# Performance work log

Hardware: AMD Instinct MI355X
Metric: run time of the kernel (lower is better)

The kernel has to match this reference:

```python
import jax, jax.numpy as jnp
import numpy as np

B, T, N = 16, 1024, 512        # batch, time tokens, neurons
DK_T, DK_S = 64, 128           # key dims (temporal, spatial)
# dim_T = N, dim_S = T, dim_value_T = N (required by cross einsum), heads = 1


def setup_inputs() -> dict:
    key = jax.random.key(0)
    ks = jax.random.split(key, 11)
    return {
        "x_T": jax.random.normal(ks[0], (B, T, N), jnp.float32),
        "x_S": jax.random.normal(ks[1], (B, N, T), jnp.float32),
        "Wq_T": jax.random.normal(ks[2], (N, DK_T), jnp.float32) * 0.05,
        "Wk_T": jax.random.normal(ks[3], (N, DK_T), jnp.float32) * 0.05,
        "Wv_T": jax.random.normal(ks[4], (N, N), jnp.float32) * 0.05,
        "Wq_S": jax.random.normal(ks[5], (T, DK_S), jnp.float32) * 0.05,
        "Wk_S": jax.random.normal(ks[6], (T, DK_S), jnp.float32) * 0.05,
        "Wout_T": jax.random.normal(ks[7], (N, N), jnp.float32) * 0.05,
        "bout_T": jax.random.normal(ks[8], (N,), jnp.float32) * 0.05,
        "bias_T": jax.random.normal(ks[9], (1, 1, 1, DK_T), jnp.float32),
        "bias_S": jax.random.normal(ks[10], (1, 1, 1, DK_S), jnp.float32),
    }


def reference(x_T, x_S, Wq_T, Wk_T, Wv_T, Wq_S, Wk_S, Wout_T, bout_T, bias_T, bias_S):
    scale_T = DK_T ** -0.5
    scale_S = DK_S ** -0.5
    # Temporal attention: tokens along time axis, heads=1 -> add h axis
    q_T = (x_T @ Wq_T)[:, None] * scale_T          # [b,1,t,dk_T]
    k_T = (x_T @ Wk_T)[:, None]                    # [b,1,t,dk_T]
    v_T = (x_T @ Wv_T)[:, None]                    # [b,1,t,n]  (dim_value_T = n)
    logits_T = jnp.einsum('bhid,bhjd->bhij', q_T + bias_T, k_T)  # [b,1,t,t]
    attn_T = jax.nn.softmax(logits_T, axis=-1)
    out_T = jnp.einsum('bhij,bhjd->bhid', attn_T, v_T)            # [b,1,t,n]
    # Spatial attention: tokens along neuron axis
    q_S = (x_S @ Wq_S)[:, None] * scale_S          # [b,1,n,dk_S]
    k_S = (x_S @ Wk_S)[:, None]                    # [b,1,n,dk_S]
    logits_S = jnp.einsum('bhid,bhjd->bhij', q_S + bias_S, k_S)   # [b,1,n,n]
    attn_S = jax.nn.softmax(logits_S, axis=-1)
    # spatial_temporal_1 cross combination: attn_S mixes the neuron axis of out_T
    out_T = jnp.einsum('bhij,bhtj->bhti', attn_S, out_T)          # [b,1,t,n]
    out_T = out_T.reshape(B, T, N)                 # 'b h t d -> b t (h d)'
    out_T = out_T @ Wout_T + bout_T                # to_out_T
    return jnp.transpose(out_T, (0, 2, 1))         # [b, n, t]
```

## Files before the change

kernel.cpp:

```cpp
#include <hip/hip_runtime.h>
#include <cstddef>

typedef short short8 __attribute__((ext_vector_type(8)));
typedef unsigned short ushortx8 __attribute__((ext_vector_type(8)));
typedef float floatx4 __attribute__((ext_vector_type(4)));

__device__ __forceinline__ unsigned int bf16_rne(float x) {
    unsigned int u = __float_as_uint(x);
    return (u + 0x7fffu + ((u >> 16) & 1u)) >> 16;
}

__device__ __forceinline__ void split4(const floatx4 v,
                                       unsigned long long& hp,
                                       unsigned long long& lp) {
    unsigned int h[4], l[4];
    #pragma unroll
    for (int j = 0; j < 4; ++j) {
        h[j] = bf16_rne(v[j]);
        float hf = __uint_as_float(h[j] << 16);
        l[j] = bf16_rne(v[j] - hf);
    }
    hp = (unsigned long long)(h[0] | (h[1] << 16)) |
         ((unsigned long long)(h[2] | (h[3] << 16)) << 32);
    lp = (unsigned long long)(l[0] | (l[1] << 16)) |
         ((unsigned long long)(l[2] | (l[3] << 16)) << 32);
}

__device__ __forceinline__ unsigned long long pack_hi4(const floatx4 v) {
    unsigned int h0 = bf16_rne(v[0]), h1 = bf16_rne(v[1]);
    unsigned int h2 = bf16_rne(v[2]), h3 = bf16_rne(v[3]);
    return (unsigned long long)(h0 | (h1 << 16)) |
           ((unsigned long long)(h2 | (h3 << 16)) << 32);
}

template<int BM, int BN, int AMODE, int BMODE, int OUTMODE, bool HASBIAS>
__global__ __launch_bounds__(256, 2)
void gemm_nt(const void* __restrict__ Ah_, const void* __restrict__ Al_,
             const void* __restrict__ Bh_, const void* __restrict__ Bl_,
             void* __restrict__ C_, void* __restrict__ Cl_,
             const float* __restrict__ bias,
             int K, int lda, int ldb, int ldc,
             long sA, long sB, long sC, float alpha, int nsplit)
{
    constexpr bool ALO = (AMODE == 1 || AMODE == 3);
    constexpr bool BLO = (BMODE == 1 || BMODE == 3);
    constexpr int LS = 40;
    __shared__ unsigned short Ash[2][BM][LS];
    __shared__ unsigned short Als[2][ALO ? BM : 1][LS];
    __shared__ unsigned short Bsh[2][BN][LS];
    __shared__ unsigned short Bls[2][BLO ? BN : 1][LS];

    const unsigned int gx = gridDim.x;
    const unsigned int nwg = gx * gridDim.y;
    unsigned int flat = blockIdx.y * gx + blockIdx.x;
    {
        unsigned int qq = nwg >> 3, rr = nwg & 7;
        unsigned int xcd = flat & 7, idx = flat >> 3;
        flat = (xcd < rr) ? (xcd * (qq + 1) + idx)
                          : (rr * (qq + 1) + (xcd - rr) * qq + idx);
    }
    const int b   = blockIdx.z;
    const int bm0 = (flat / gx) * BM;
    const int bn0 = (flat % gx) * BN;
    const int tid  = threadIdx.x;
    const int lane = tid & 63;
    const int wid  = tid >> 6;
    const int wr = wid >> 1, wc = wid & 1;
    constexpr int WM = BM / 2, WN = BN / 2;
    constexpr int FM = WM / 16, FN = WN / 16;
    floatx4 acc[FM][FN] = {};
    const int l15  = lane & 15;
    const int koff = (lane >> 4) * 8;

    constexpr int ACHF = BM * 32 / 4, NAF0 = (ACHF + 255) / 256;
    constexpr int ACHH = BM * 32 / 8, NAH0 = (ACHH + 255) / 256;
    constexpr int BCHF = BN * 32 / 4, NBF0 = (BCHF + 255) / 256;
    constexpr int BCHH = BN * 32 / 8, NBH0 = (BCHH + 255) / 256;
    constexpr int NAF = (AMODE <= 1) ? NAF0 : 1;
    constexpr int NAH = (AMODE >= 2) ? NAH0 : 1;
    constexpr int NBF = (BMODE <= 1) ? NBF0 : 1;
    constexpr int NBH = (BMODE >= 2) ? NBH0 : 1;
    floatx4  aF[NAF], bF[NBF];
    ushortx8 aH[NAH], aL[NAH], bH[NBH], bL[NBH];

    auto loadA = [&](int k0) {
        if (AMODE <= 1) {
            const float* A = (const float*)Ah_ + (long)b * sA;
            #pragma unroll
            for (int i = 0; i < NAF; ++i) {
                int idx = i * 256 + tid;
                if (ACHF % 256 == 0 || idx < ACHF) {
                    int flatc = idx * 4;
                    int r = flatc >> 5, c = flatc & 31;
                    aF[i] = *(const floatx4*)(A + (long)(bm0 + r) * lda + k0 + c);
                }
            }
        } else {
            const unsigned short* A  = (const unsigned short*)Ah_ + (long)b * sA;
            const unsigned short* Al = (const unsigned short*)Al_ + (long)b * sA;
            #pragma unroll
            for (int i = 0; i < NAH; ++i) {
                int idx = i * 256 + tid;
                if (ACHH % 256 == 0 || idx < ACHH) {
                    int flatc = idx * 8;
                    int r = flatc >> 5, c = flatc & 31;
                    aH[i] = *(const ushortx8*)(A + (long)(bm0 + r) * lda + k0 + c);
                    if (AMODE == 3)
                        aL[i] = *(const ushortx8*)(Al + (long)(bm0 + r) * lda + k0 + c);
                }
            }
        }
    };
    auto loadB = [&](int k0) {
        if (BMODE <= 1) {
            const float* Bp = (const float*)Bh_ + (long)b * sB;
            #pragma unroll
            for (int i = 0; i < NBF; ++i) {
                int idx = i * 256 + tid;
                if (BCHF % 256 == 0 || idx < BCHF) {
                    int flatc = idx * 4;
                    int r = flatc >> 5, c = flatc & 31;
                    bF[i] = *(const floatx4*)(Bp + (long)(bn0 + r) * ldb + k0 + c);
                }
            }
        } else {
            const unsigned short* Bp = (const unsigned short*)Bh_ + (long)b * sB;
            const unsigned short* Bl = (const unsigned short*)Bl_ + (long)b * sB;
            #pragma unroll
            for (int i = 0; i < NBH; ++i) {
                int idx = i * 256 + tid;
                if (BCHH % 256 == 0 || idx < BCHH) {
                    int flatc = idx * 8;
                    int r = flatc >> 5, c = flatc & 31;
                    bH[i] = *(const ushortx8*)(Bp + (long)(bn0 + r) * ldb + k0 + c);
                    if (BMODE == 3)
                        bL[i] = *(const ushortx8*)(Bl + (long)(bn0 + r) * ldb + k0 + c);
                }
            }
        }
    };
    auto writeA = [&](int bf) {
        if (AMODE <= 1) {
            #pragma unroll
            for (int i = 0; i < NAF; ++i) {
                int idx = i * 256 + tid;
                if (ACHF % 256 == 0 || idx < ACHF) {
                    int flatc = idx * 4;
                    int r = flatc >> 5, c = flatc & 31;
                    if (AMODE == 1) {
                        unsigned long long hp, lp; split4(aF[i], hp, lp);
                        *(unsigned long long*)&Ash[bf][r][c] = hp;
                        *(unsigned long long*)&Als[bf][r][c] = lp;
                    } else {
                        *(unsigned long long*)&Ash[bf][r][c] = pack_hi4(aF[i]);
                    }
                }
            }
        } else {
            #pragma unroll
            for (int i = 0; i < NAH; ++i) {
                int idx = i * 256 + tid;
                if (ACHH % 256 == 0 || idx < ACHH) {
                    int flatc = idx * 8;
                    int r = flatc >> 5, c = flatc & 31;
                    *(ushortx8*)&Ash[bf][r][c] = aH[i];
                    if (AMODE == 3) *(ushortx8*)&Als[bf][r][c] = aL[i];
                }
            }
        }
    };
    auto writeB = [&](int bf) {
        if (BMODE <= 1) {
            #pragma unroll
            for (int i = 0; i < NBF; ++i) {
                int idx = i * 256 + tid;
                if (BCHF % 256 == 0 || idx < BCHF) {
                    int flatc = idx * 4;
                    int r = flatc >> 5, c = flatc & 31;
                    if (BMODE == 1) {
                        unsigned long long hp, lp; split4(bF[i], hp, lp);
                        *(unsigned long long*)&Bsh[bf][r][c] = hp;
                        *(unsigned long long*)&Bls[bf][r][c] = lp;
                    } else {
                        *(unsigned long long*)&Bsh[bf][r][c] = pack_hi4(bF[i]);
                    }
                }
            }
        } else {
            #pragma unroll
            for (int i = 0; i < NBH; ++i) {
                int idx = i * 256 + tid;
                if (BCHH % 256 == 0 || idx < BCHH) {
                    int flatc = idx * 8;
                    int r = flatc >> 5, c = flatc & 31;
                    *(ushortx8*)&Bsh[bf][r][c] = bH[i];
                    if (BMODE == 3) *(ushortx8*)&Bls[bf][r][c] = bL[i];
                }
            }
        }
    };
    auto compute = [&](int bf) {
        short8 ah[FM], al[FM], bh[FN], bl[FN];
        #pragma unroll
        for (int mi = 0; mi < FM; ++mi) {
            ah[mi] = *(const short8*)&Ash[bf][wr * WM + mi * 16 + l15][koff];
            if (ALO) al[mi] = *(const short8*)&Als[bf][wr * WM + mi * 16 + l15][koff];
        }
        #pragma unroll
        for (int ni = 0; ni < FN; ++ni) {
            bh[ni] = *(const short8*)&Bsh[bf][wc * WN + ni * 16 + l15][koff];
            if (BLO) bl[ni] = *(const short8*)&Bls[bf][wc * WN + ni * 16 + l15][koff];
        }
        #pragma unroll
        for (int mi = 0; mi < FM; ++mi)
            #pragma unroll
            for (int ni = 0; ni < FN; ++ni) {
                if (ALO)
                    acc[mi][ni] = __builtin_amdgcn_mfma_f32_16x16x32_bf16(
                        al[mi], bh[ni], acc[mi][ni], 0, 0, 0);
                if (BLO)
                    acc[mi][ni] = __builtin_amdgcn_mfma_f32_16x16x32_bf16(
                        ah[mi], bl[ni], acc[mi][ni], 0, 0, 0);
                acc[mi][ni] = __builtin_amdgcn_mfma_f32_16x16x32_bf16(
                    ah[mi], bh[ni], acc[mi][ni], 0, 0, 0);
            }
    };

    loadA(0); loadB(0);
    writeA(0); writeB(0);
    __syncthreads();
    int cur = 0;
    for (int k0 = 32; k0 < K; k0 += 32) {
        loadA(k0); loadB(k0);
        compute(cur);
        writeA(cur ^ 1); writeB(cur ^ 1);
        __syncthreads();
        cur ^= 1;
    }
    compute(cur);

    const int rq = (lane >> 4) * 4;
    #pragma unroll
    for (int mi = 0; mi < FM; ++mi) {
        #pragma unroll
        for (int ni = 0; ni < FN; ++ni) {
            int gm = bm0 + wr * WM + mi * 16 + rq;
            int gn = bn0 + wc * WN + ni * 16 + l15;
            float ae = (gn < nsplit) ? alpha : 1.0f;
            float be = 0.f;
            if (HASBIAS) be = (gn < nsplit) ? bias[gn] : 0.0f;
            float vals[4];
            #pragma unroll
            for (int j = 0; j < 4; ++j) vals[j] = acc[mi][ni][j] * ae + be;
            if (OUTMODE == 0) {
                float* C = (float*)C_ + (long)b * sC;
                #pragma unroll
                for (int j = 0; j < 4; ++j) C[(long)(gm + j) * ldc + gn] = vals[j];
            } else if (OUTMODE == 1) {
                float* C = (float*)C_ + (long)b * sC;
                floatx4 o;
                #pragma unroll
                for (int j = 0; j < 4; ++j) o[j] = vals[j];
                *(floatx4*)(C + (long)gn * ldc + gm) = o;
            } else if (OUTMODE == 2) {
                unsigned short* Ch = (unsigned short*)C_ + (long)b * sC;
                unsigned short* Cl = (unsigned short*)Cl_ + (long)b * sC;
                #pragma unroll
                for (int j = 0; j < 4; ++j) {
                    unsigned int h = bf16_rne(vals[j]);
                    float hf = __uint_as_float(h << 16);
                    unsigned int lo = bf16_rne(vals[j] - hf);
                    Ch[(long)(gm + j) * ldc + gn] = (unsigned short)h;
                    Cl[(long)(gm + j) * ldc + gn] = (unsigned short)lo;
                }
            } else {
                unsigned short* Ch = (unsigned short*)C_ + (long)b * sC;
                #pragma unroll
                for (int j = 0; j < 4; ++j)
                    Ch[(long)(gm + j) * ldc + gn] = (unsigned short)bf16_rne(vals[j]);
            }
        }
    }
}

template<int COLS, int DK, int LDQK>
__global__ __launch_bounds__(256, 2)
void qk_softmax(const unsigned short* __restrict__ qk_h,
                const unsigned short* __restrict__ qk_l,
                unsigned short* __restrict__ P)
{
    constexpr int WCOLS = COLS / 4;
    constexpr int FN = WCOLS / 16;
    constexpr int QPAD = DK + 24;
    __shared__ unsigned short Qh[32][QPAD];
    __shared__ unsigned short Ql[32][QPAD];
    __shared__ float red[32][4];
    __shared__ unsigned short Pl[32][COLS + 8];

    const int b  = blockIdx.y;
    const int q0 = blockIdx.x * 32;
    const long rowBase = (long)b * COLS;
    const int tid = threadIdx.x;
    const int lane = tid & 63, wid = tid >> 6;
    const int l15 = lane & 15, g = lane >> 4;
    const int koff = g * 8;

    constexpr int QCH = DK / 8;
    for (int i = tid; i < 32 * QCH; i += 256) {
        int r = i / QCH, c = (i % QCH) * 8;
        *(ushortx8*)&Qh[r][c] = *(const ushortx8*)(qk_h + (rowBase + q0 + r) * LDQK + c);
        *(ushortx8*)&Ql[r][c] = *(const ushortx8*)(qk_l + (rowBase + q0 + r) * LDQK + c);
    }
    __syncthreads();

    floatx4 acc[2][FN] = {};
    const unsigned short* kh = qk_h + rowBase * LDQK + DK;
    const unsigned short* kl = qk_l + rowBase * LDQK + DK;

    #pragma unroll
    for (int kk = 0; kk < DK; kk += 32) {
        short8 ah[2], al[2];
        #pragma unroll
        for (int mi = 0; mi < 2; ++mi) {
            ah[mi] = *(const short8*)&Qh[mi * 16 + l15][kk + koff];
            al[mi] = *(const short8*)&Ql[mi * 16 + l15][kk + koff];
        }
        #pragma unroll
        for (int ni = 0; ni < FN; ++ni) {
            long krow = wid * WCOLS + ni * 16 + l15;
            short8 bh = *(const short8*)(kh + krow * LDQK + kk + koff);
            short8 bl = *(const short8*)(kl + krow * LDQK + kk + koff);
            #pragma unroll
            for (int mi = 0; mi < 2; ++mi) {
                acc[mi][ni] = __builtin_amdgcn_mfma_f32_16x16x32_bf16(al[mi], bh, acc[mi][ni], 0, 0, 0);
                acc[mi][ni] = __builtin_amdgcn_mfma_f32_16x16x32_bf16(ah[mi], bl, acc[mi][ni], 0, 0, 0);
                acc[mi][ni] = __builtin_amdgcn_mfma_f32_16x16x32_bf16(ah[mi], bh, acc[mi][ni], 0, 0, 0);
            }
        }
    }

    float pm[2][4];
    #pragma unroll
    for (int mi = 0; mi < 2; ++mi)
        #pragma unroll
        for (int j = 0; j < 4; ++j) {
            float m = acc[mi][0][j];
            #pragma unroll
            for (int ni = 1; ni < FN; ++ni) m = fmaxf(m, acc[mi][ni][j]);
            pm[mi][j] = m;
        }
    #pragma unroll
    for (int msk = 1; msk < 16; msk <<= 1) {
        #pragma unroll
        for (int mi = 0; mi < 2; ++mi)
            #pragma unroll
            for (int j = 0; j < 4; ++j)
                pm[mi][j] = fmaxf(pm[mi][j], __shfl_xor(pm[mi][j], msk));
    }
    if (l15 == 0) {
        #pragma unroll
        for (int mi = 0; mi < 2; ++mi)
            #pragma unroll
            for (int j = 0; j < 4; ++j) red[mi * 16 + g * 4 + j][wid] = pm[mi][j];
    }
    __syncthreads();
    float rm[2][4];
    #pragma unroll
    for (int mi = 0; mi < 2; ++mi)
        #pragma unroll
        for (int j = 0; j < 4; ++j) {
            const float* r4 = red[mi * 16 + g * 4 + j];
            rm[mi][j] = fmaxf(fmaxf(r4[0], r4[1]), fmaxf(r4[2], r4[3]));
        }
    __syncthreads();

    float ps[2][4] = {};
    #pragma unroll
    for (int mi = 0; mi < 2; ++mi)
        #pragma unroll
        for (int ni = 0; ni < FN; ++ni)
            #pragma unroll
            for (int j = 0; j < 4; ++j) {
                float e = __expf(acc[mi][ni][j] - rm[mi][j]);
                acc[mi][ni][j] = e;
                ps[mi][j] += e;
            }
    #pragma unroll
    for (int msk = 1; msk < 16; msk <<= 1) {
        #pragma unroll
        for (int mi = 0; mi < 2; ++mi)
            #pragma unroll
            for (int j = 0; j < 4; ++j)
                ps[mi][j] += __shfl_xor(ps[mi][j], msk);
    }
    if (l15 == 0) {
        #pragma unroll
        for (int mi = 0; mi < 2; ++mi)
            #pragma unroll
            for (int j = 0; j < 4; ++j) red[mi * 16 + g * 4 + j][wid] = ps[mi][j];
    }
    __syncthreads();
    float inv[2][4];
    #pragma unroll
    for (int mi = 0; mi < 2; ++mi)
        #pragma unroll
        for (int j = 0; j < 4; ++j) {
            const float* r4 = red[mi * 16 + g * 4 + j];
            inv[mi][j] = 1.0f / (r4[0] + r4[1] + r4[2] + r4[3]);
        }

    #pragma unroll
    for (int mi = 0; mi < 2; ++mi)
        #pragma unroll
        for (int ni = 0; ni < FN; ++ni)
            #pragma unroll
            for (int j = 0; j < 4; ++j)
                Pl[mi * 16 + g * 4 + j][wid * WCOLS + ni * 16 + l15] =
                    (unsigned short)bf16_rne(acc[mi][ni][j] * inv[mi][j]);
    __syncthreads();

    constexpr int PCH = COLS / 8;
    for (int i = tid; i < 32 * PCH; i += 256) {
        int r = i / PCH, c = (i % PCH) * 8;
        *(ushortx8*)(P + (rowBase + q0 + r) * COLS + c) = *(const ushortx8*)&Pl[r][c];
    }
}

__global__ __launch_bounds__(256)
void transpose_split(const float* __restrict__ in,
                     unsigned short* __restrict__ outH,
                     unsigned short* __restrict__ outL,
                     int R, int C, int rowOff, int ldo)
{
    __shared__ float tile[32][33];
    const int tc = blockIdx.x * 32, tr = blockIdx.y * 32;
    const int x = threadIdx.x, y = threadIdx.y;
    #pragma unroll
    for (int i = 0; i < 32; i += 8)
        tile[y + i][x] = in[(long)(tr + y + i) * C + tc + x];
    __syncthreads();
    #pragma unroll
    for (int i = 0; i < 32; i += 8) {
        float v = tile[x][y + i];
        unsigned int h = bf16_rne(v);
        float hf = __uint_as_float(h << 16);
        unsigned int lo = bf16_rne(v - hf);
        long idx = (long)(tc + y + i + rowOff) * ldo + tr + x;
        outH[idx] = (unsigned short)h;
        outL[idx] = (unsigned short)lo;
    }
}

extern "C" void kernel_launch(void* const* d_in, const int* in_sizes, int n_in,
                              void* d_out, int out_size, void* d_ws, size_t ws_size,
                              hipStream_t stream)
{
    (void)in_sizes; (void)n_in; (void)out_size; (void)ws_size;
    const float* x_T    = (const float*)d_in[0];
    const float* x_S    = (const float*)d_in[1];
    const float* Wq_T   = (const float*)d_in[2];
    const float* Wk_T   = (const float*)d_in[3];
    const float* Wv_T   = (const float*)d_in[4];
    const float* Wq_S   = (const float*)d_in[5];
    const float* Wk_S   = (const float*)d_in[6];
    const float* Wout_T = (const float*)d_in[7];
    const float* bout_T = (const float*)d_in[8];
    const float* bias_T = (const float*)d_in[9];
    const float* bias_S = (const float*)d_in[10];
    float* out = (float*)d_out;

    constexpr int B = 16, T = 1024, N = 512, DKT = 64, DKS = 128;
    typedef unsigned short us;

    char* w = (char*)d_ws;
    size_t off = 0;
    auto alloc = [&](size_t bytes) { char* p = w + off; off = (off + bytes + 255) & ~(size_t)255; return p; };
    us* wqkT_h = (us*)alloc(128 * 512 * 2);
    us* wqkT_l = (us*)alloc(128 * 512 * 2);
    us* wvt_h  = (us*)alloc(512 * 512 * 2);
    us* wvt_l  = (us*)alloc(512 * 512 * 2);
    us* wqks_h = (us*)alloc(256 * 1024 * 2);
    us* wqks_l = (us*)alloc(256 * 1024 * 2);
    us* wout_h = (us*)alloc(512 * 512 * 2);
    us* wout_l = (us*)alloc(512 * 512 * 2);
    us* qk_h   = (us*)alloc((size_t)16384 * 128 * 2);
    us* qk_l   = (us*)alloc((size_t)16384 * 128 * 2);
    us* P_T    = (us*)alloc((size_t)B * T * T * 2);
    us* P_S    = (us*)alloc((size_t)B * N * N * 2);
    us* vT_h   = (us*)alloc((size_t)B * N * T * 2);
    us* vT_l   = (us*)alloc((size_t)B * N * T * 2);
    us* outT_h = (us*)alloc((size_t)B * T * N * 2);
    us* outT_l = (us*)alloc((size_t)B * T * N * 2);
    us* out2_h = vT_h;
    us* out2_l = vT_l;

    const float scale_T = 0.125f;
    const float scale_S = 0.088388347648318447f;
    const int BIG = 1 << 30;

    dim3 tb(32, 8);
    transpose_split<<<dim3(2, 16),  tb, 0, stream>>>(Wq_T,   wqkT_h, wqkT_l, 512, 64,   0, 512);
    transpose_split<<<dim3(2, 16),  tb, 0, stream>>>(Wk_T,   wqkT_h, wqkT_l, 512, 64,  64, 512);
    transpose_split<<<dim3(16, 16), tb, 0, stream>>>(Wv_T,   wvt_h,  wvt_l,  512, 512,  0, 512);
    transpose_split<<<dim3(4, 32),  tb, 0, stream>>>(Wq_S,   wqks_h, wqks_l, 1024, 128, 0, 1024);
    transpose_split<<<dim3(4, 32),  tb, 0, stream>>>(Wk_S,   wqks_h, wqks_l, 1024, 128, 128, 1024);
    transpose_split<<<dim3(16, 16), tb, 0, stream>>>(Wout_T, wout_h, wout_l, 512, 512,  0, 512);

    gemm_nt<32, 128, 1, 3, 2, true><<<dim3(1, 512, 1), 256, 0, stream>>>(
        x_T, nullptr, wqkT_h, wqkT_l, qk_h, qk_l, bias_T,
        512, 512, 512, 128, 0, 0, 0, scale_T, 64);
    gemm_nt<128, 128, 3, 0, 3, false><<<dim3(8, 4, B), 256, 0, stream>>>(
        wvt_h, wvt_l, x_T, nullptr, vT_h, nullptr, nullptr,
        512, 512, 512, 1024, 0, (long)T * N, (long)N * T, 1.0f, 0);
    qk_softmax<1024, 64, 128><<<dim3(32, 16), 256, 0, stream>>>(qk_h, qk_l, P_T);
    gemm_nt<128, 128, 2, 2, 2, false><<<dim3(4, 8, B), 256, 0, stream>>>(
        P_T, nullptr, vT_h, nullptr, outT_h, outT_l, nullptr,
        1024, 1024, 1024, 512, (long)T * T, (long)N * T, (long)T * N, 1.0f, 0);

    gemm_nt<32, 128, 1, 3, 2, true><<<dim3(2, 256, 1), 256, 0, stream>>>(
        x_S, nullptr, wqks_h, wqks_l, qk_h, qk_l, bias_S,
        1024, 1024, 1024, 256, 0, 0, 0, scale_S, 128);
    qk_softmax<512, 128, 256><<<dim3(16, 16), 256, 0, stream>>>(qk_h, qk_l, P_S);
    gemm_nt<128, 128, 3, 2, 2, false><<<dim3(4, 8, B), 256, 0, stream>>>(
        outT_h, outT_l, P_S, nullptr, out2_h, out2_l, nullptr,
        512, 512, 512, 512, (long)T * N, (long)N * N, (long)T * N, 1.0f, 0);
    gemm_nt<128, 128, 3, 2, 1, true><<<dim3(4, 8, B), 256, 0, stream>>>(
        out2_h, out2_l, wout_h, nullptr, out, nullptr, bout_T,
        512, 512, 512, 1024, (long)T * N, 0, (long)N * T, 1.0f, BIG);
}
```

Baseline: 221.8 us.

## Reassociate spatial mixing with output projection, pre-split inputs, shrink GEMM tiles

Transposes P_S in the softmax epilogue and first multiplies it with Wout_T, a per-batch 512x512 product. Applying that merged matrix to out_T removes one full T×N×N GEMM per batch. It also adds a convert_split pass that turns x_T and x_S into bf16 hi/lo arrays once, so the projection GEMMs read split data instead of converting inside the loads. Tiles shrink to 64x64 or 64x128, occupancy is raised to 4 blocks per SM, and the batch index is folded into a flat 2D grid, all to give more waves. The merged matrix M1t is stored only as the bf16 high part, which may lower accuracy.

```diff
diff --git a/kernel.cpp b/kernel.cpp
--- a/kernel.cpp
+++ b/kernel.cpp
@@ -3,6 +3,7 @@
 
 typedef short short8 __attribute__((ext_vector_type(8)));
 typedef unsigned short ushortx8 __attribute__((ext_vector_type(8)));
+typedef unsigned short ushortx4 __attribute__((ext_vector_type(4)));
 typedef float floatx4 __attribute__((ext_vector_type(4)));
 
 __device__ __forceinline__ unsigned int bf16_rne(float x) {
@@ -33,14 +34,36 @@
            ((unsigned long long)(h2 | (h3 << 16)) << 32);
 }
 
+__global__ __launch_bounds__(256)
+void convert_split(const float* __restrict__ in, long n,
+                   unsigned short* __restrict__ H, unsigned short* __restrict__ L)
+{
+    long n4 = n >> 2;
+    for (long i = (long)blockIdx.x * 256 + threadIdx.x; i < n4;
+         i += (long)gridDim.x * 256) {
+        long e = i << 2;
+        floatx4 v = *(const floatx4*)(in + e);
+        ushortx4 h4, l4;
+        #pragma unroll
+        for (int j = 0; j < 4; ++j) {
+            unsigned int h = bf16_rne(v[j]);
+            float hf = __uint_as_float(h << 16);
+            h4[j] = (unsigned short)h;
+            l4[j] = (unsigned short)bf16_rne(v[j] - hf);
+        }
+        *(ushortx4*)(H + e) = h4;
+        *(ushortx4*)(L + e) = l4;
+    }
+}
+
 template<int BM, int BN, int AMODE, int BMODE, int OUTMODE, bool HASBIAS>
-__global__ __launch_bounds__(256, 2)
+__global__ __launch_bounds__(256, 4)
 void gemm_nt(const void* __restrict__ Ah_, const void* __restrict__ Al_,
              const void* __restrict__ Bh_, const void* __restrict__ Bl_,
              void* __restrict__ C_, void* __restrict__ Cl_,
              const float* __restrict__ bias,
              int K, int lda, int ldb, int ldc,
-             long sA, long sB, long sC, float alpha, int nsplit)
+             long sA, long sB, long sC, float alpha, int nsplit, int mtiles)
 {
     constexpr bool ALO = (AMODE == 1 || AMODE == 3);
     constexpr bool BLO = (BMODE == 1 || BMODE == 3);
@@ -59,9 +82,11 @@
         flat = (xcd < rr) ? (xcd * (qq + 1) + idx)
                           : (rr * (qq + 1) + (xcd - rr) * qq + idx);
     }
-    const int b   = blockIdx.z;
-    const int bm0 = (flat / gx) * BM;
-    const int bn0 = (flat % gx) * BN;
+    const unsigned int perb = gx * (unsigned int)mtiles;
+    const int b   = flat / perb;
+    const unsigned int rm = flat % perb;
+    const int bm0 = (rm / gx) * BM;
+    const int bn0 = (rm % gx) * BN;
     const int tid  = threadIdx.x;
     const int lane = tid & 63;
     const int wid  = tid >> 6;
@@ -90,8 +115,7 @@
             for (int i = 0; i < NAF; ++i) {
                 int idx = i * 256 + tid;
                 if (ACHF % 256 == 0 || idx < ACHF) {
-                    int flatc = idx * 4;
-                    int r = flatc >> 5, c = flatc & 31;
+                    int fc = idx * 4; int r = fc >> 5, c = fc & 31;
                     aF[i] = *(const floatx4*)(A + (long)(bm0 + r) * lda + k0 + c);
                 }
             }
@@ -102,8 +126,7 @@
             for (int i = 0; i < NAH; ++i) {
                 int idx = i * 256 + tid;
                 if (ACHH % 256 == 0 || idx < ACHH) {
-                    int flatc = idx * 8;
-                    int r = flatc >> 5, c = flatc & 31;
+                    int fc = idx * 8; int r = fc >> 5, c = fc & 31;
                     aH[i] = *(const ushortx8*)(A + (long)(bm0 + r) * lda + k0 + c);
                     if (AMODE == 3)
                         aL[i] = *(const ushortx8*)(Al + (long)(bm0 + r) * lda + k0 + c);
@@ -118,8 +141,7 @@
             for (int i = 0; i < NBF; ++i) {
                 int idx = i * 256 + tid;
                 if (BCHF % 256 == 0 || idx < BCHF) {
-                    int flatc = idx * 4;
-                    int r = flatc >> 5, c = flatc & 31;
+                    int fc = idx * 4; int r = fc >> 5, c = fc & 31;
                     bF[i] = *(const floatx4*)(Bp + (long)(bn0 + r) * ldb + k0 + c);
                 }
             }
@@ -130,8 +152,7 @@
             for (int i = 0; i < NBH; ++i) {
                 int idx = i * 256 + tid;
                 if (BCHH % 256 == 0 || idx < BCHH) {
-                    int flatc = idx * 8;
-                    int r = flatc >> 5, c = flatc & 31;
+                    int fc = idx * 8; int r = fc >> 5, c = fc & 31;
                     bH[i] = *(const ushortx8*)(Bp + (long)(bn0 + r) * ldb + k0 + c);
                     if (BMODE == 3)
                         bL[i] = *(const ushortx8*)(Bl + (long)(bn0 + r) * ldb + k0 + c);
@@ -145,8 +166,7 @@
             for (int i = 0; i < NAF; ++i) {
                 int idx = i * 256 + tid;
                 if (ACHF % 256 == 0 || idx < ACHF) {
-                    int flatc = idx * 4;
-                    int r = flatc >> 5, c = flatc & 31;
+                    int fc = idx * 4; int r = fc >> 5, c = fc & 31;
                     if (AMODE == 1) {
                         unsigned long long hp, lp; split4(aF[i], hp, lp);
                         *(unsigned long long*)&Ash[bf][r][c] = hp;
@@ -161,8 +181,7 @@
             for (int i = 0; i < NAH; ++i) {
                 int idx = i * 256 + tid;
                 if (ACHH % 256 == 0 || idx < ACHH) {
-                    int flatc = idx * 8;
-                    int r = flatc >> 5, c = flatc & 31;
+                    int fc = idx * 8; int r = fc >> 5, c = fc & 31;
                     *(ushortx8*)&Ash[bf][r][c] = aH[i];
                     if (AMODE == 3) *(ushortx8*)&Als[bf][r][c] = aL[i];
                 }
@@ -175,8 +194,7 @@
             for (int i = 0; i < NBF; ++i) {
                 int idx = i * 256 + tid;
                 if (BCHF % 256 == 0 || idx < BCHF) {
-                    int flatc = idx * 4;
-                    int r = flatc >> 5, c = flatc & 31;
+                    int fc = idx * 4; int r = fc >> 5, c = fc & 31;
                     if (BMODE == 1) {
                         unsigned long long hp, lp; split4(bF[i], hp, lp);
                         *(unsigned long long*)&Bsh[bf][r][c] = hp;
@@ -191,8 +209,7 @@
             for (int i = 0; i < NBH; ++i) {
                 int idx = i * 256 + tid;
                 if (BCHH % 256 == 0 || idx < BCHH) {
-                    int flatc = idx * 8;
-                    int r = flatc >> 5, c = flatc & 31;
+                    int fc = idx * 8; int r = fc >> 5, c = fc & 31;
                     *(ushortx8*)&Bsh[bf][r][c] = bH[i];
                     if (BMODE == 3) *(ushortx8*)&Bls[bf][r][c] = bL[i];
                 }
@@ -283,7 +300,7 @@
     }
 }
 
-template<int COLS, int DK, int LDQK>
+template<int COLS, int DK, int LDQK, bool TRANSP>
 __global__ __launch_bounds__(256, 2)
 void qk_softmax(const unsigned short* __restrict__ qk_h,
                 const unsigned short* __restrict__ qk_l,
@@ -419,10 +436,21 @@
                     (unsigned short)bf16_rne(acc[mi][ni][j] * inv[mi][j]);
     __syncthreads();
 
-    constexpr int PCH = COLS / 8;
-    for (int i = tid; i < 32 * PCH; i += 256) {
-        int r = i / PCH, c = (i % PCH) * 8;
-        *(ushortx8*)(P + (rowBase + q0 + r) * COLS + c) = *(const ushortx8*)&Pl[r][c];
+    if (TRANSP) {
+        for (int i = tid; i < COLS * 4; i += 256) {
+            int c = i >> 2;
+            int rc = (i & 3) * 8;
+            ushortx8 v;
+            #pragma unroll
+            for (int s = 0; s < 8; ++s) v[s] = Pl[rc + s][c];
+            *(ushortx8*)(P + (rowBase + c) * COLS + q0 + rc) = v;
+        }
+    } else {
+        constexpr int PCH = COLS / 8;
+        for (int i = tid; i < 32 * PCH; i += 256) {
+            int r = i / PCH, c = (i % PCH) * 8;
+            *(ushortx8*)(P + (rowBase + q0 + r) * COLS + c) = *(const ushortx8*)&Pl[r][c];
+        }
     }
 }
 
@@ -486,17 +514,19 @@
     us* qk_h   = (us*)alloc((size_t)16384 * 128 * 2);
     us* qk_l   = (us*)alloc((size_t)16384 * 128 * 2);
     us* P_T    = (us*)alloc((size_t)B * T * T * 2);
-    us* P_S    = (us*)alloc((size_t)B * N * N * 2);
+    us* P_St   = (us*)alloc((size_t)B * N * N * 2);
     us* vT_h   = (us*)alloc((size_t)B * N * T * 2);
     us* vT_l   = (us*)alloc((size_t)B * N * T * 2);
     us* outT_h = (us*)alloc((size_t)B * T * N * 2);
     us* outT_l = (us*)alloc((size_t)B * T * N * 2);
-    us* out2_h = vT_h;
-    us* out2_l = vT_l;
+    us* x_h    = (us*)alloc((size_t)16384 * 512 * 2);
+    us* x_l    = (us*)alloc((size_t)16384 * 512 * 2);
+    us* M1t_h  = vT_l;
 
     const float scale_T = 0.125f;
     const float scale_S = 0.088388347648318447f;
     const int BIG = 1 << 30;
+    const long XE = (long)16384 * 512;
 
     dim3 tb(32, 8);
     transpose_split<<<dim3(2, 16),  tb, 0, stream>>>(Wq_T,   wqkT_h, wqkT_l, 512, 64,   0, 512);
@@ -506,25 +536,27 @@
     transpose_split<<<dim3(4, 32),  tb, 0, stream>>>(Wk_S,   wqks_h, wqks_l, 1024, 128, 128, 1024);
     transpose_split<<<dim3(16, 16), tb, 0, stream>>>(Wout_T, wout_h, wout_l, 512, 512,  0, 512);
 
-    gemm_nt<32, 128, 1, 3, 2, true><<<dim3(1, 512, 1), 256, 0, stream>>>(
-        x_T, nullptr, wqkT_h, wqkT_l, qk_h, qk_l, bias_T,
-        512, 512, 512, 128, 0, 0, 0, scale_T, 64);
-    gemm_nt<128, 128, 3, 0, 3, false><<<dim3(8, 4, B), 256, 0, stream>>>(
-        wvt_h, wvt_l, x_T, nullptr, vT_h, nullptr, nullptr,
-        512, 512, 512, 1024, 0, (long)T * N, (long)N * T, 1.0f, 0);
-    qk_softmax<1024, 64, 128><<<dim3(32, 16), 256, 0, stream>>>(qk_h, qk_l, P_T);
-    gemm_nt<128, 128, 2, 2, 2, false><<<dim3(4, 8, B), 256, 0, stream>>>(
+    convert_split<<<2048, 256, 0, stream>>>(x_T, XE, x_h, x_l);
+    gemm_nt<64, 64, 3, 3, 2, true><<<dim3(2, 256), 256, 0, stream>>>(
+        x_h, x_l, wqkT_h, wqkT_l, qk_h, qk_l, bias_T,
+        512, 512, 512, 128, 0, 0, 0, scale_T, 64, 256);
+    gemm_nt<64, 128, 3, 2, 3, false><<<dim3(8, 8 * B), 256, 0, stream>>>(
+        wvt_h, wvt_l, x_h, nullptr, vT_h, nullptr, nullptr,
+        512, 512, 512, 1024, 0, (long)T * N, (long)N * T, 1.0f, 0, 8);
+    qk_softmax<1024, 64, 128, false><<<dim3(32, 16), 256, 0, stream>>>(qk_h, qk_l, P_T);
+    gemm_nt<64, 128, 2, 2, 2, false><<<dim3(4, 16 * B), 256, 0, stream>>>(
         P_T, nullptr, vT_h, nullptr, outT_h, outT_l, nullptr,
-        1024, 1024, 1024, 512, (long)T * T, (long)N * T, (long)T * N, 1.0f, 0);
-
-    gemm_nt<32, 128, 1, 3, 2, true><<<dim3(2, 256, 1), 256, 0, stream>>>(
-        x_S, nullptr, wqks_h, wqks_l, qk_h, qk_l, bias_S,
-        1024, 1024, 1024, 256, 0, 0, 0, scale_S, 128);
-    qk_softmax<512, 128, 256><<<dim3(16, 16), 256, 0, stream>>>(qk_h, qk_l, P_S);
-    gemm_nt<128, 128, 3, 2, 2, false><<<dim3(4, 8, B), 256, 0, stream>>>(
-        outT_h, outT_l, P_S, nullptr, out2_h, out2_l, nullptr,
-        512, 512, 512, 512, (long)T * N, (long)N * N, (long)T * N, 1.0f, 0);
-    gemm_nt<128, 128, 3, 2, 1, true><<<dim3(4, 8, B), 256, 0, stream>>>(
-        out2_h, out2_l, wout_h, nullptr, out, nullptr, bout_T,
-        512, 512, 512, 1024, (long)T * N, 0, (long)N * T, 1.0f, BIG);
-}
+        1024, 1024, 1024, 512, (long)T * T, (long)N * T, (long)T * N, 1.0f, 0, 16);
+
+    convert_split<<<2048, 256, 0, stream>>>(x_S, XE, x_h, x_l);
+    gemm_nt<64, 64, 3, 3, 2, true><<<dim3(4, 128), 256, 0, stream>>>(
+        x_h, x_l, wqks_h, wqks_l, qk_h, qk_l, bias_S,
+        1024, 1024, 1024, 256, 0, 0, 0, scale_S, 128, 128);
+    qk_softmax<512, 128, 256, true><<<dim3(16, 16), 256, 0, stream>>>(qk_h, qk_l, P_St);
+    gemm_nt<64, 128, 3, 2, 3, false><<<dim3(4, 8 * B), 256, 0, stream>>>(
+        wout_h, wout_l, P_St, nullptr, M1t_h, nullptr, nullptr,
+        512, 512, 512, 512, 0, (long)N * N, (long)N * N, 1.0f, 0, 8);
+    gemm_nt<64, 128, 3, 2, 1, true><<<dim3(4, 16 * B), 256, 0, stream>>>(
+        outT_h, outT_l, M1t_h, nullptr, out, nullptr, bout_T,
+        512, 512, 512, 1024, (long)T * N, (long)N * N, (long)N * T, 1.0f, BIG, 16);
+}
```

Measured after the change: 223.9 us. About the same (+1.0%).
